# Kernel optimization log

Hardware: AMD Instinct MI355X
Metric: run time of the kernel (lower is better)

The kernel has to match this reference:

```python
import jax, jax.numpy as jnp
import numpy as np
import math

GRID = 32          # config.grid_size
DIM = 256          # sparse_head_dim = n_embd * mlp_internal_dim_multiplier // n_head
B, H = 8, 8        # batch, n_head
N = GRID * GRID    # tokens = grid_size^2


def get_freqs_2d(h, w, dim, theta=10000.0):
    """2D RoPE angles; returns (cos, sin) each of shape (h*w, dim//2)."""
    dim_half = dim // 2
    inv = 1.0 / theta ** (np.arange(0, dim_half, 2).astype(np.float32) / dim_half)
    fx = np.outer(np.arange(w, dtype=np.float32), inv)   # (w, dim_half//2)
    fy = np.outer(np.arange(h, dtype=np.float32), inv)   # (h, dim_half//2)
    fx_grid = np.broadcast_to(fx[None, :, :], (h, w, fx.shape[1]))
    fy_grid = np.broadcast_to(fy[:, None, :], (h, w, fy.shape[1]))
    ang = np.concatenate([fx_grid, fy_grid], axis=-1).reshape(h * w, dim_half)
    return jnp.asarray(np.cos(ang)), jnp.asarray(np.sin(ang))


def apply_rotary(x, cos, sin):
    # x: (B,H,N,D) viewed as complex pairs along last dim; complex multiply by e^{i*ang}
    xr = x.reshape(*x.shape[:-1], -1, 2)
    x0, x1 = xr[..., 0], xr[..., 1]          # (B,H,N,D/2)
    out_re = x0 * cos - x1 * sin
    out_im = x0 * sin + x1 * cos
    return jnp.stack([out_re, out_im], axis=-1).reshape(x.shape)


def setup_inputs() -> dict:
    key = jax.random.key(0)
    k1, k2, k3 = jax.random.split(key, 3)
    shape = (B, H, N, DIM)
    return {
        "Q": jax.random.normal(k1, shape, dtype=jnp.float32),
        "K": jax.random.normal(k2, shape, dtype=jnp.float32),
        "V": jax.random.normal(k3, shape, dtype=jnp.float32),
    }


def reference(Q, K, V):
    cos, sin = get_freqs_2d(GRID, GRID, DIM)  # (N, DIM/2) each, broadcast over B,H
    QR = apply_rotary(Q, cos, sin)
    KR = apply_rotary(K, cos, sin)
    scores = jnp.einsum('bhnd,bhmd->bhnm', QR, KR) / math.sqrt(QR.shape[-1])
    attn = jax.nn.softmax(scores, axis=-1)
    return jnp.einsum('bhnm,bhmd->bhnd', attn, V)
```

## Files before the change

kernel.cpp:

```cpp
#include <hip/hip_runtime.h>
#include <hip/hip_bf16.h>
#include <cstdint>

#define BH     64
#define NTOK   1024
#define DDIM   256
#define QT     128
#define KTILE  32
#define NITER  (NTOK / KTILE)
#define PP     40

typedef __bf16 bf16x8 __attribute__((ext_vector_type(8)));
typedef float  f32x4  __attribute__((ext_vector_type(4)));

__device__ __forceinline__ unsigned short f2bf(float f) {
    __bf16 b = (__bf16)f;
    return __builtin_bit_cast(unsigned short, b);
}
__device__ __forceinline__ float bf2f(unsigned short u) {
    return __builtin_bit_cast(float, ((unsigned int)u) << 16);
}
__device__ __forceinline__ unsigned int pack2(float lo, float hi) {
    return (unsigned int)f2bf(lo) | ((unsigned int)f2bf(hi) << 16);
}

typedef const __attribute__((address_space(1))) unsigned int* gas_t;
typedef __attribute__((address_space(3))) unsigned int* las_t;
__device__ __forceinline__ void gload16(const void* g, void* l) {
    __builtin_amdgcn_global_load_lds((gas_t)g, (las_t)l, 16, 0, 0);
}

#define ANG_C    (13.287712379549449f / 64.0f)
#define SM_SCALE (1.4426950408889634f / 16.0f)

__global__ __launch_bounds__(256) void prep(const float* __restrict__ K,
                                            const float* __restrict__ V,
                                            unsigned short* __restrict__ KR,
                                            unsigned short* __restrict__ VT) {
    __shared__ unsigned short tile[64 * 264];
    int tid = threadIdx.x;
    if (blockIdx.x < 8192) {
        int gid = blockIdx.x * 256 + tid;
        int chunk = gid & 31;
        int t = (gid >> 5) & (NTOK - 1);
        float x = (float)(t & 31), y = (float)(t >> 5);
        const float4 a = *(const float4*)(K + (size_t)gid * 8);
        const float4 b = *(const float4*)(K + (size_t)gid * 8 + 4);
        float f[8] = {a.x, a.y, a.z, a.w, b.x, b.y, b.z, b.w};
        unsigned int o[4];
#pragma unroll
        for (int p = 0; p < 4; ++p) {
            int j = chunk * 4 + p;
            float pos = (j < 64) ? x : y;
            float inv = __builtin_exp2f(-(float)(j & 63) * ANG_C);
            float s, c;
            __sincosf(pos * inv, &s, &c);
            float x0 = f[2 * p], x1 = f[2 * p + 1];
            o[p] = pack2(x0 * c - x1 * s, x0 * s + x1 * c);
        }
        uint4 ov; ov.x = o[0]; ov.y = o[1]; ov.z = o[2]; ov.w = o[3];
        *(uint4*)(KR + (size_t)gid * 8) = ov;
        return;
    }
    int vb = blockIdx.x - 8192;
    int bh = vb >> 4;
    int tbase = (vb & 15) * 64;
    const float* src = V + ((size_t)bh * NTOK + tbase) * DDIM;
#pragma unroll
    for (int i = 0; i < 8; ++i) {
        int flat = i * 2048 + tid * 8;
        int tl = flat >> 8, col = flat & 255;
        const float4 a = *(const float4*)(src + (size_t)tl * DDIM + col);
        const float4 b = *(const float4*)(src + (size_t)tl * DDIM + col + 4);
        uint4 ov;
        ov.x = pack2(a.x, a.y); ov.y = pack2(a.z, a.w);
        ov.z = pack2(b.x, b.y); ov.w = pack2(b.z, b.w);
        *(uint4*)(tile + tl * 264 + col) = ov;
    }
    __syncthreads();
    unsigned short* dst = VT + (size_t)bh * ((size_t)DDIM * NTOK) + tbase;
#pragma unroll
    for (int i = 0; i < 8; ++i) {
        int task = i * 256 + tid;
        int d = task >> 3, tq = task & 7;
        unsigned int o[4];
#pragma unroll
        for (int k = 0; k < 4; ++k) {
            unsigned short lo = tile[(tq * 8 + 2 * k    ) * 264 + d];
            unsigned short hi = tile[(tq * 8 + 2 * k + 1) * 264 + d];
            o[k] = (unsigned int)lo | ((unsigned int)hi << 16);
        }
        uint4 ov; ov.x = o[0]; ov.y = o[1]; ov.z = o[2]; ov.w = o[3];
        *(uint4*)(dst + (size_t)d * NTOK + tq * 8) = ov;
    }
}

__global__ __launch_bounds__(512, 4) void flash_attn(
        const float* __restrict__ Q,
        const unsigned short* __restrict__ KR,
        const unsigned short* __restrict__ VTg,
        float* __restrict__ Out) {
    __shared__ unsigned short KT[2][KTILE * DDIM];
    __shared__ unsigned short VT[2][DDIM * KTILE];
    __shared__ unsigned short PB[8][16 * PP];

    const int tid = threadIdx.x;
    const int wave = tid >> 6, lane = tid & 63;
    const int g = lane >> 4, l15 = lane & 15;
    const int b = blockIdx.x;
    const int bh = (b & 7) + ((b >> 6) << 3);
    const int qbase = ((b >> 3) & 7) * QT;

    const unsigned short* krB = KR + (size_t)bh * ((size_t)NTOK * DDIM);
    const unsigned short* vtB = VTg + (size_t)bh * ((size_t)DDIM * NTOK);

    bf16x8 qfrag[8];
    {
        const int qtok = qbase + wave * 16 + l15;
        const float x = (float)(qtok & 31), y = (float)(qtok >> 5);
        const float* qrow = Q + ((size_t)bh * NTOK + qtok) * DDIM;
#pragma unroll
        for (int kk = 0; kk < 8; ++kk) {
            const float4 a = *(const float4*)(qrow + kk * 32 + g * 8);
            const float4 b2 = *(const float4*)(qrow + kk * 32 + g * 8 + 4);
            float f[8] = {a.x, a.y, a.z, a.w, b2.x, b2.y, b2.z, b2.w};
            unsigned int po[4];
#pragma unroll
            for (int p = 0; p < 4; ++p) {
                int j = kk * 16 + g * 4 + p;
                float pos = (j < 64) ? x : y;
                float inv = __builtin_exp2f(-(float)(j & 63) * ANG_C);
                float s, c;
                __sincosf(pos * inv, &s, &c);
                float x0 = f[2 * p], x1 = f[2 * p + 1];
                po[p] = pack2(x0 * c - x1 * s, x0 * s + x1 * c);
            }
            uint4 pk; pk.x = po[0]; pk.y = po[1]; pk.z = po[2]; pk.w = po[3];
            qfrag[kk] = __builtin_bit_cast(bf16x8, pk);
        }
    }
    asm volatile("s_waitcnt vmcnt(0)" ::: "memory");

    f32x4 o[16];
    const f32x4 zero4 = {0.f, 0.f, 0.f, 0.f};
#pragma unroll
    for (int nt = 0; nt < 16; ++nt) o[nt] = zero4;
    float lsum[4] = {0.f, 0.f, 0.f, 0.f};

    int kOff[2], vOff[2];
#pragma unroll
    for (int j = 0; j < 2; ++j) {
        int f = wave * 128 + j * 64 + lane;
        int rf = f >> 5, sf = f & 31;
        kOff[j] = rf * 256 + ((sf ^ (rf & 7)) * 8);
        int gI = f >> 3, s = f & 7;
        int ss = s ^ (gI & 7);
        int d = gI * 2 + (ss >> 2), c = ss & 3;
        vOff[j] = d * 1024 + c * 8;
    }
    const int kx = l15 & 7;
    const int vrd = (l15 >> 1) * 64 +
                    (((((l15 & 1) << 2) | g) ^ ((l15 >> 1) & 7)) * 8);

#pragma unroll
    for (int j = 0; j < 2; ++j)
        gload16(krB + kOff[j], &KT[0][wave * 1024 + j * 512]);
#pragma unroll
    for (int j = 0; j < 2; ++j)
        gload16(vtB + vOff[j], &VT[0][wave * 1024 + j * 512]);

    for (int it = 0; it < NITER; ++it) {
        const int cur = it & 1;
        if (it + 1 < NITER) {
            const int kb = (it + 1) * KTILE;
            const unsigned short* krT = krB + (size_t)kb * DDIM;
            const unsigned short* vtT = vtB + kb;
            const int nxt = cur ^ 1;
#pragma unroll
            for (int j = 0; j < 2; ++j)
                gload16(krT + kOff[j], &KT[nxt][wave * 1024 + j * 512]);
#pragma unroll
            for (int j = 0; j < 2; ++j)
                gload16(vtT + vOff[j], &VT[nxt][wave * 1024 + j * 512]);
            asm volatile("s_waitcnt vmcnt(4)" ::: "memory");
        } else {
            asm volatile("s_waitcnt vmcnt(0)" ::: "memory");
        }
        __builtin_amdgcn_s_barrier();

        f32x4 sc0 = zero4, sc1 = zero4;
        const unsigned short* ktb = KT[cur];
        __builtin_amdgcn_s_setprio(1);
#pragma unroll
        for (int kk = 0; kk < 8; ++kk) {
            const int sl = (((kk << 2) + g) ^ kx) * 8;
            bf16x8 b0 = *(const bf16x8*)(ktb + l15 * 256 + sl);
            bf16x8 b1 = *(const bf16x8*)(ktb + (16 + l15) * 256 + sl);
            sc0 = __builtin_amdgcn_mfma_f32_16x16x32_bf16(qfrag[kk], b0, sc0, 0, 0, 0);
            sc1 = __builtin_amdgcn_mfma_f32_16x16x32_bf16(qfrag[kk], b1, sc1, 0, 0, 0);
        }
        __builtin_amdgcn_s_setprio(0);

        unsigned short* pbw = &PB[wave][0];
#pragma unroll
        for (int r = 0; r < 4; ++r) {
            float p0 = __builtin_exp2f(sc0[r] * SM_SCALE);
            float p1 = __builtin_exp2f(sc1[r] * SM_SCALE);
            unsigned short b0 = f2bf(p0), b1 = f2bf(p1);
            pbw[(4 * g + r) * PP + l15] = b0;
            pbw[(4 * g + r) * PP + 16 + l15] = b1;
            lsum[r] += bf2f(b0) + bf2f(b1);
        }
        bf16x8 af = *(const bf16x8*)(pbw + l15 * PP + g * 8);

        const unsigned short* vtb = VT[cur];
        __builtin_amdgcn_s_setprio(1);
#pragma unroll
        for (int nt = 0; nt < 16; ++nt) {
            bf16x8 vb = *(const bf16x8*)(vtb + nt * 512 + vrd);
            o[nt] = __builtin_amdgcn_mfma_f32_16x16x32_bf16(af, vb, o[nt], 0, 0, 0);
        }
        __builtin_amdgcn_s_setprio(0);

        asm volatile("s_waitcnt lgkmcnt(0)" ::: "memory");
        __builtin_amdgcn_s_barrier();
    }

#pragma unroll
    for (int r = 0; r < 4; ++r) {
        float s = lsum[r];
        s += __shfl_xor(s, 1);
        s += __shfl_xor(s, 2);
        s += __shfl_xor(s, 4);
        s += __shfl_xor(s, 8);
        float rl = 1.0f / s;
        float* orow =
            Out + ((size_t)bh * NTOK + qbase + wave * 16 + 4 * g + r) * DDIM;
#pragma unroll
        for (int nt = 0; nt < 16; ++nt)
            orow[nt * 16 + l15] = o[nt][r] * rl;
    }
}

extern "C" void kernel_launch(void* const* d_in, const int* in_sizes, int n_in,
                              void* d_out, int out_size, void* d_ws, size_t ws_size,
                              hipStream_t stream) {
    const float* Q = (const float*)d_in[0];
    const float* K = (const float*)d_in[1];
    const float* V = (const float*)d_in[2];
    unsigned short* KR = (unsigned short*)d_ws;
    unsigned short* VT = KR + (size_t)BH * NTOK * DDIM;
    float* O = (float*)d_out;

    prep<<<8192 + BH * (NTOK / 64), 256, 0, stream>>>(K, V, KR, VT);
    flash_attn<<<BH * (NTOK / QT), 512, 0, stream>>>(Q, KR, VT, O);
}
```

Baseline: 360.9 us.

## Switch attention to 32x32x16 MFMA with 4 waves of 32 query rows

The flash attention kernel now uses 32x32x16 bf16 MFMA tiles, and each of 4 waves owns 32 query rows instead of 8 waves owning 16. LDS fragment loads, the softmax P staging layout, the V swizzle and the row reductions are rewritten to match. Each wave now reuses every K and V fragment across twice as many query rows, which cuts LDS read traffic and the MFMA instruction count. In exchange, per-wave register pressure is higher (16 Q fragments and 8 accumulators of 16 floats each), and halving the threads per block lowers occupancy.

Measured after the change: 349.0 us. -3.3%, faster.

```diff
diff --git a/kernel.cpp b/kernel.cpp
--- a/kernel.cpp
+++ b/kernel.cpp
@@ -12,6 +12,7 @@
 
 typedef __bf16 bf16x8 __attribute__((ext_vector_type(8)));
 typedef float  f32x4  __attribute__((ext_vector_type(4)));
+typedef float  f32x16 __attribute__((ext_vector_type(16)));
 
 __device__ __forceinline__ unsigned short f2bf(float f) {
     __bf16 b = (__bf16)f;
@@ -95,18 +96,18 @@
     }
 }
 
-__global__ __launch_bounds__(512, 4) void flash_attn(
+__global__ __launch_bounds__(256, 2) void flash_attn(
         const float* __restrict__ Q,
         const unsigned short* __restrict__ KR,
         const unsigned short* __restrict__ VTg,
         float* __restrict__ Out) {
     __shared__ unsigned short KT[2][KTILE * DDIM];
-    __shared__ unsigned short VT[2][DDIM * KTILE];
-    __shared__ unsigned short PB[8][16 * PP];
+    __shared__ unsigned short VTl[2][DDIM * KTILE];
+    __shared__ unsigned short PB[4][32 * PP];
 
     const int tid = threadIdx.x;
     const int wave = tid >> 6, lane = tid & 63;
-    const int g = lane >> 4, l15 = lane & 15;
+    const int l31 = lane & 31, h = lane >> 5;
     const int b = blockIdx.x;
     const int bh = (b & 7) + ((b >> 6) << 3);
     const int qbase = ((b >> 3) & 7) * QT;
@@ -114,20 +115,20 @@
     const unsigned short* krB = KR + (size_t)bh * ((size_t)NTOK * DDIM);
     const unsigned short* vtB = VTg + (size_t)bh * ((size_t)DDIM * NTOK);
 
-    bf16x8 qfrag[8];
+    bf16x8 qfrag[16];
     {
-        const int qtok = qbase + wave * 16 + l15;
+        const int qtok = qbase + wave * 32 + l31;
         const float x = (float)(qtok & 31), y = (float)(qtok >> 5);
         const float* qrow = Q + ((size_t)bh * NTOK + qtok) * DDIM;
 #pragma unroll
-        for (int kk = 0; kk < 8; ++kk) {
-            const float4 a = *(const float4*)(qrow + kk * 32 + g * 8);
-            const float4 b2 = *(const float4*)(qrow + kk * 32 + g * 8 + 4);
+        for (int cc = 0; cc < 16; ++cc) {
+            const float4 a = *(const float4*)(qrow + cc * 16 + h * 8);
+            const float4 b2 = *(const float4*)(qrow + cc * 16 + h * 8 + 4);
             float f[8] = {a.x, a.y, a.z, a.w, b2.x, b2.y, b2.z, b2.w};
             unsigned int po[4];
 #pragma unroll
             for (int p = 0; p < 4; ++p) {
-                int j = kk * 16 + g * 4 + p;
+                int j = cc * 8 + h * 4 + p;
                 float pos = (j < 64) ? x : y;
                 float inv = __builtin_exp2f(-(float)(j & 63) * ANG_C);
                 float s, c;
@@ -136,38 +137,37 @@
                 po[p] = pack2(x0 * c - x1 * s, x0 * s + x1 * c);
             }
             uint4 pk; pk.x = po[0]; pk.y = po[1]; pk.z = po[2]; pk.w = po[3];
-            qfrag[kk] = __builtin_bit_cast(bf16x8, pk);
+            qfrag[cc] = __builtin_bit_cast(bf16x8, pk);
         }
     }
     asm volatile("s_waitcnt vmcnt(0)" ::: "memory");
 
-    f32x4 o[16];
-    const f32x4 zero4 = {0.f, 0.f, 0.f, 0.f};
-#pragma unroll
-    for (int nt = 0; nt < 16; ++nt) o[nt] = zero4;
-    float lsum[4] = {0.f, 0.f, 0.f, 0.f};
-
-    int kOff[2], vOff[2];
-#pragma unroll
-    for (int j = 0; j < 2; ++j) {
-        int f = wave * 128 + j * 64 + lane;
+    f32x16 o[8] = {};
+    float lsum[16] = {};
+
+    int kOff[4], vOff[4];
+#pragma unroll
+    for (int j = 0; j < 4; ++j) {
+        int f = wave * 256 + j * 64 + lane;
         int rf = f >> 5, sf = f & 31;
         kOff[j] = rf * 256 + ((sf ^ (rf & 7)) * 8);
-        int gI = f >> 3, s = f & 7;
-        int ss = s ^ (gI & 7);
-        int d = gI * 2 + (ss >> 2), c = ss & 3;
-        vOff[j] = d * 1024 + c * 8;
-    }
-    const int kx = l15 & 7;
-    const int vrd = (l15 >> 1) * 64 +
-                    (((((l15 & 1) << 2) | g) ^ ((l15 >> 1) & 7)) * 8);
-
-#pragma unroll
-    for (int j = 0; j < 2; ++j)
-        gload16(krB + kOff[j], &KT[0][wave * 1024 + j * 512]);
-#pragma unroll
-    for (int j = 0; j < 2; ++j)
-        gload16(vtB + vOff[j], &VT[0][wave * 1024 + j * 512]);
+        int d0 = ((f >> 2) ^ (f >> 4)) & 1;
+        int dv = ((f >> 3) << 1) | d0;
+        int cv = (f & 3) ^ (dv & 3);
+        vOff[j] = dv * NTOK + cv * 8;
+    }
+    const int kx = l31 & 7;
+    const int vrd0 = ((4 * l31 + 0 + h) ^ kx) * 8;
+    const int vrd1 = ((4 * l31 + 2 + h) ^ kx) * 8;
+
+#pragma unroll
+    for (int j = 0; j < 4; ++j)
+        gload16(krB + kOff[j], &KT[0][wave * 2048 + j * 512]);
+#pragma unroll
+    for (int j = 0; j < 4; ++j)
+        gload16(vtB + vOff[j], &VTl[0][wave * 2048 + j * 512]);
+
+    unsigned short* pbw = &PB[wave][0];
 
     for (int it = 0; it < NITER; ++it) {
         const int cur = it & 1;
@@ -177,48 +177,46 @@
             const unsigned short* vtT = vtB + kb;
             const int nxt = cur ^ 1;
 #pragma unroll
-            for (int j = 0; j < 2; ++j)
-                gload16(krT + kOff[j], &KT[nxt][wave * 1024 + j * 512]);
-#pragma unroll
-            for (int j = 0; j < 2; ++j)
-                gload16(vtT + vOff[j], &VT[nxt][wave * 1024 + j * 512]);
-            asm volatile("s_waitcnt vmcnt(4)" ::: "memory");
+            for (int j = 0; j < 4; ++j)
+                gload16(krT + kOff[j], &KT[nxt][wave * 2048 + j * 512]);
+#pragma unroll
+            for (int j = 0; j < 4; ++j)
+                gload16(vtT + vOff[j], &VTl[nxt][wave * 2048 + j * 512]);
+            asm volatile("s_waitcnt vmcnt(8)" ::: "memory");
         } else {
             asm volatile("s_waitcnt vmcnt(0)" ::: "memory");
         }
         __builtin_amdgcn_s_barrier();
 
-        f32x4 sc0 = zero4, sc1 = zero4;
+        f32x16 sc = {};
         const unsigned short* ktb = KT[cur];
         __builtin_amdgcn_s_setprio(1);
 #pragma unroll
-        for (int kk = 0; kk < 8; ++kk) {
-            const int sl = (((kk << 2) + g) ^ kx) * 8;
-            bf16x8 b0 = *(const bf16x8*)(ktb + l15 * 256 + sl);
-            bf16x8 b1 = *(const bf16x8*)(ktb + (16 + l15) * 256 + sl);
-            sc0 = __builtin_amdgcn_mfma_f32_16x16x32_bf16(qfrag[kk], b0, sc0, 0, 0, 0);
-            sc1 = __builtin_amdgcn_mfma_f32_16x16x32_bf16(qfrag[kk], b1, sc1, 0, 0, 0);
+        for (int cc = 0; cc < 16; ++cc) {
+            const int sl = ((2 * cc + h) ^ kx) * 8;
+            bf16x8 kb_ = *(const bf16x8*)(ktb + l31 * 256 + sl);
+            sc = __builtin_amdgcn_mfma_f32_32x32x16_bf16(qfrag[cc], kb_, sc, 0, 0, 0);
         }
         __builtin_amdgcn_s_setprio(0);
 
-        unsigned short* pbw = &PB[wave][0];
-#pragma unroll
-        for (int r = 0; r < 4; ++r) {
-            float p0 = __builtin_exp2f(sc0[r] * SM_SCALE);
-            float p1 = __builtin_exp2f(sc1[r] * SM_SCALE);
-            unsigned short b0 = f2bf(p0), b1 = f2bf(p1);
-            pbw[(4 * g + r) * PP + l15] = b0;
-            pbw[(4 * g + r) * PP + 16 + l15] = b1;
-            lsum[r] += bf2f(b0) + bf2f(b1);
-        }
-        bf16x8 af = *(const bf16x8*)(pbw + l15 * PP + g * 8);
-
-        const unsigned short* vtb = VT[cur];
+#pragma unroll
+        for (int r = 0; r < 16; ++r) {
+            float p = __builtin_exp2f(sc[r] * SM_SCALE);
+            unsigned short pb = f2bf(p);
+            pbw[((r & 3) + 8 * (r >> 2) + 4 * h) * PP + l31] = pb;
+            lsum[r] += bf2f(pb);
+        }
+        bf16x8 pa0 = *(const bf16x8*)(pbw + l31 * PP + h * 8);
+        bf16x8 pa1 = *(const bf16x8*)(pbw + l31 * PP + 16 + h * 8);
+
+        const unsigned short* vtb = VTl[cur];
         __builtin_amdgcn_s_setprio(1);
 #pragma unroll
-        for (int nt = 0; nt < 16; ++nt) {
-            bf16x8 vb = *(const bf16x8*)(vtb + nt * 512 + vrd);
-            o[nt] = __builtin_amdgcn_mfma_f32_16x16x32_bf16(af, vb, o[nt], 0, 0, 0);
+        for (int nt = 0; nt < 8; ++nt) {
+            bf16x8 v0 = *(const bf16x8*)(vtb + nt * 1024 + vrd0);
+            bf16x8 v1 = *(const bf16x8*)(vtb + nt * 1024 + vrd1);
+            o[nt] = __builtin_amdgcn_mfma_f32_32x32x16_bf16(pa0, v0, o[nt], 0, 0, 0);
+            o[nt] = __builtin_amdgcn_mfma_f32_32x32x16_bf16(pa1, v1, o[nt], 0, 0, 0);
         }
         __builtin_amdgcn_s_setprio(0);
 
@@ -227,18 +225,20 @@
     }
 
 #pragma unroll
-    for (int r = 0; r < 4; ++r) {
+    for (int r = 0; r < 16; ++r) {
         float s = lsum[r];
         s += __shfl_xor(s, 1);
         s += __shfl_xor(s, 2);
         s += __shfl_xor(s, 4);
         s += __shfl_xor(s, 8);
+        s += __shfl_xor(s, 16);
         float rl = 1.0f / s;
+        const int row = (r & 3) + 8 * (r >> 2) + 4 * h;
         float* orow =
-            Out + ((size_t)bh * NTOK + qbase + wave * 16 + 4 * g + r) * DDIM;
-#pragma unroll
-        for (int nt = 0; nt < 16; ++nt)
-            orow[nt * 16 + l15] = o[nt][r] * rl;
+            Out + ((size_t)bh * NTOK + qbase + wave * 32 + row) * DDIM;
+#pragma unroll
+        for (int nt = 0; nt < 8; ++nt)
+            orow[nt * 32 + l31] = o[nt][r] * rl;
     }
 }
 
@@ -253,5 +253,5 @@
     float* O = (float*)d_out;
 
     prep<<<8192 + BH * (NTOK / 64), 256, 0, stream>>>(K, V, KR, VT);
-    flash_attn<<<BH * (NTOK / QT), 512, 0, stream>>>(Q, KR, VT, O);
-}
+    flash_attn<<<BH * (NTOK / QT), 256, 0, stream>>>(Q, KR, VT, O);
+}
```
